# Performance work log

Measured on AMD Instinct MI355X. Metric: run time of the kernel, lower is better.

The kernel has to match this reference:

```python
import jax, jax.numpy as jnp
import numpy as np

N = 8192        # num nodes (bs in the original docstring)
D_IN = 512      # input feature dim
HEADS = 8
DPH = 512 // HEADS  # size_per_head = hidden_size // num_heads
EDGE_P = 0.01   # adjacency density


def setup_inputs() -> dict:
    key = jax.random.key(0)
    k1, k2, k3 = jax.random.split(key, 3)
    H = jax.random.normal(k1, (N, D_IN), dtype=jnp.float32)
    # dense 0/1 adjacency, as passed to the layer before tf.sparse.from_dense
    adj = (jax.random.uniform(k2, (N, N)) < EDGE_P).astype(jnp.float32)
    # Glorot-uniform per-head projection kernels, stacked: (HEADS, D_IN, DPH)
    limit = float(np.sqrt(6.0 / (D_IN + DPH)))
    W = jax.random.uniform(k3, (HEADS, D_IN, DPH), jnp.float32, -limit, limit)
    b = jnp.zeros((HEADS, DPH), jnp.float32)
    return {"H": H, "adj": adj, "W": W, "b": b}


def reference(H, adj, W, b):
    # Per-head dense projection: H_ = H @ W_h  -> (HEADS, N, DPH)
    H_ = jnp.einsum('nd,hde->hne', H, W)
    # NOTE: the original layer computes a sparse sigmoid/softmax attention
    # (f1 + f2^T over adj) but never uses it: head_output uses raw adj.
    # Aggregation: adj @ H_ per head, plus bias; activation = tf.identity.
    out = jnp.einsum('nm,hme->hne', adj, H_) + b[:, None, :]  # (HEADS, N, DPH)
    # Concat heads along feature axis (head 0 first) -> (N, HEADS*DPH)
    return jnp.transpose(out, (1, 0, 2)).reshape(H.shape[0], HEADS * DPH)
```

## Files before the change

### kernel.cpp

```cpp
#include <hip/hip_runtime.h>
#include <hip/hip_bf16.h>

typedef __attribute__((ext_vector_type(8))) short short8;
typedef __attribute__((ext_vector_type(4))) float floatx4;
typedef __attribute__((ext_vector_type(4))) uint uintx4;

#define GN 8192
#define GD 512
#define GEMM_BLOCKS 512

static __device__ __forceinline__ ushort bf16bits(float x) {
  __hip_bfloat16 h = __float2bfloat16(x);
  return *(ushort*)&h;
}
static __device__ __forceinline__ float bf16f(uint u16) {
  return __uint_as_float(u16 << 16);
}

typedef __attribute__((address_space(1))) const void g1_void;
typedef __attribute__((address_space(3))) void l3_void;
static __device__ __forceinline__ void gl_lds16(const void* g, void* l) {
  __builtin_amdgcn_global_load_lds((g1_void*)g, (l3_void*)l, 16, 0, 0);
}

__global__ void detect_kernel(const uint* __restrict__ H, const uint* __restrict__ W,
                              const uint* __restrict__ adj, const uint* __restrict__ b,
                              int* __restrict__ flags, float* __restrict__ bias) {
  __shared__ int cH, cW, cA, cB;
  const int t = threadIdx.x;
  if (t == 0) { cH = 0; cW = 0; cA = 0; cB = 0; }
  __syncthreads();
  { const uint e = (H[t] >> 7) & 0xFFu; if (e >= 100u && e <= 140u) atomicAdd(&cH, 1); }
  { const uint e = (W[t] >> 7) & 0xFFu; if (e >= 100u && e <= 140u) atomicAdd(&cW, 1); }
  for (int i = t; i < 4096; i += 256)
    if ((adj[i] & 0xFFFFu) == 0x3F80u) atomicAdd(&cA, 1);
  if (b[t] != 0u) atomicAdd(&cB, 1);
  __syncthreads();
  const int hb = cH > 128, wb = cW > 128, ab = cA > 0;
  if (t == 0) { flags[0] = hb; flags[1] = wb; flags[2] = ab; }
  if (cB == 0) {
    bias[t] = 0.0f; bias[t + 256] = 0.0f;
  } else if (wb) {
    const ushort* bs = (const ushort*)b;
    bias[t] = bf16f(bs[t]); bias[t + 256] = bf16f(bs[t + 256]);
  } else {
    const float* bf = (const float*)b;
    bias[t] = bf[t]; bias[t + 256] = bf[t + 256];
  }
}

#define BM 128
#define BN 64
#define BK 64
#define LDK 72

#define SMEM_BYTES (BM * LDK * 2 + BN * LDK * 2)

__global__ __launch_bounds__(256) void proj_kernel(
    const void* __restrict__ Hv, const void* __restrict__ Wv,
    ushort* __restrict__ HPt, const int* __restrict__ flags) {
  __shared__ __align__(16) unsigned char smem[SMEM_BYTES];
  ushort* sA = (ushort*)smem;
  ushort* sB = (ushort*)(smem + BM * LDK * 2);
  const int tid = threadIdx.x;
  const int hb = flags[0];
  const int wb = flags[1];
  const int bn = blockIdx.x & 7;
  const int bm = blockIdx.x >> 3;
  const int m0 = bm * BM;
  const int lane = tid & 63;
  const int w = tid >> 6;
  const int wr = w >> 1, wc = w & 1;
  const int l15 = lane & 15, q = lane >> 4;

  floatx4 acc[4][2];
#pragma unroll
  for (int i = 0; i < 4; i++)
#pragma unroll
    for (int j = 0; j < 2; j++) acc[i][j] = (floatx4)0.0f;

  for (int k0 = 0; k0 < GD; k0 += BK) {
    __syncthreads();
    if (hb) {
      const ushort* H16 = (const ushort*)Hv;
      const int r = tid >> 3;
      const int kc = (tid & 7) * 8;
#pragma unroll
      for (int p = 0; p < 4; p++) {
        const int row = r + p * 32;
        const uint4 v = *(const uint4*)(H16 + (size_t)(m0 + row) * GD + k0 + kc);
        *(uint4*)(sA + row * LDK + kc) = v;
      }
    } else {
      const float* H32 = (const float*)Hv;
      const int r0 = tid >> 4;
      const int kc = (tid & 15) * 4;
#pragma unroll
      for (int p = 0; p < 8; p++) {
        const int row = r0 + p * 16;
        const float4 v = *(const float4*)(H32 + (size_t)(m0 + row) * GD + k0 + kc);
        ushort4 o;
        o.x = bf16bits(v.x); o.y = bf16bits(v.y);
        o.z = bf16bits(v.z); o.w = bf16bits(v.w);
        *(ushort4*)(sA + row * LDK + kc) = o;
      }
    }
    if (wb) {
      const ushort* Wh = (const ushort*)Wv + (size_t)bn * (512 * 64);
      const int kk = tid >> 3;
      const int e0 = (tid & 7) * 8;
#pragma unroll
      for (int p = 0; p < 2; p++) {
        const int k = kk + p * 32;
        const uint4 v = *(const uint4*)(Wh + (size_t)(k0 + k) * 64 + e0);
        const ushort* pv = (const ushort*)&v;
#pragma unroll
        for (int j = 0; j < 8; j++) sB[(e0 + j) * LDK + k] = pv[j];
      }
    } else {
      const float* Wh = (const float*)Wv + (size_t)bn * (512 * 64);
      const int kk = tid >> 4;
      const int e0 = (tid & 15) * 4;
#pragma unroll
      for (int p = 0; p < 4; p++) {
        const int k = kk + p * 16;
        const float4 v = *(const float4*)(Wh + (size_t)(k0 + k) * 64 + e0);
        sB[(e0 + 0) * LDK + k] = bf16bits(v.x);
        sB[(e0 + 1) * LDK + k] = bf16bits(v.y);
        sB[(e0 + 2) * LDK + k] = bf16bits(v.z);
        sB[(e0 + 3) * LDK + k] = bf16bits(v.w);
      }
    }
    __syncthreads();
#pragma unroll
    for (int kq = 0; kq < 2; kq++) {
      short8 af[4], bfv[2];
#pragma unroll
      for (int mt = 0; mt < 4; mt++)
        af[mt] = *(const short8*)(sA + (wr * 64 + mt * 16 + l15) * LDK + kq * 32 + q * 8);
#pragma unroll
      for (int ct = 0; ct < 2; ct++)
        bfv[ct] = *(const short8*)(sB + (wc * 32 + ct * 16 + l15) * LDK + kq * 32 + q * 8);
#pragma unroll
      for (int mt = 0; mt < 4; mt++)
#pragma unroll
        for (int ct = 0; ct < 2; ct++)
          acc[mt][ct] = __builtin_amdgcn_mfma_f32_16x16x32_bf16(
              af[mt], bfv[ct], acc[mt][ct], 0, 0, 0);
    }
  }
#pragma unroll
  for (int mt = 0; mt < 4; mt++)
#pragma unroll
    for (int ct = 0; ct < 2; ct++) {
      const int col = bn * 64 + wc * 32 + ct * 16 + l15;
      const int rowb = m0 + wr * 64 + mt * 16 + q * 4;
      ushort4 o;
      o.x = bf16bits(acc[mt][ct][0]);
      o.y = bf16bits(acc[mt][ct][1]);
      o.z = bf16bits(acc[mt][ct][2]);
      o.w = bf16bits(acc[mt][ct][3]);
      *(ushort4*)(HPt + (size_t)col * GN + rowb) = o;
    }
}

#define ABM 64
#define ABK 64
#define AKCH 4096
#define ALDA 72

__global__ __launch_bounds__(512) void agg_kernel(
    const void* __restrict__ adjv, const ushort* __restrict__ HPt,
    float* __restrict__ pbuf, const int* __restrict__ flags) {
  __shared__ __align__(16) ushort sA[ABM * ALDA];
  __shared__ __align__(16) ushort sB[GD * 64];
  const int ab = flags[2];
  const int bid = blockIdx.x;
  const int kch = bid & 1;
  const int m0 = (bid >> 1) * ABM;
  const size_t kb = (size_t)kch * AKCH;
  const int tid = threadIdx.x;
  const int lane = tid & 63, w = tid >> 6;
  const int l15 = lane & 15, q = lane >> 4;

  floatx4 acc[4][4];
#pragma unroll
  for (int i = 0; i < 4; i++)
#pragma unroll
    for (int j = 0; j < 4; j++) acc[i][j] = (floatx4)0.0f;

  const int be0 = w * 8 + (lane >> 3);
  const int bkc = (lane & 7) * 8;

  for (int k0 = 0; k0 < AKCH; k0 += ABK) {
    __syncthreads();
#pragma unroll
    for (int p = 0; p < 8; p++) {
      const int e = p * 64 + be0;
      gl_lds16(HPt + (size_t)e * GN + kb + k0 + bkc,
               sB + (size_t)(p * 64 + w * 8) * 64);
    }
    if (ab) {
      const ushort* adj16 = (const ushort*)adjv;
      const int n = tid >> 3;
      const int kc = (tid & 7) * 8;
      const uintx4 v = __builtin_nontemporal_load(
          (const uintx4*)(adj16 + (size_t)(m0 + n) * GN + kb + k0 + kc));
      *(uintx4*)(sA + n * ALDA + kc) = v;
    } else {
      const float* adj32 = (const float*)adjv;
      const int n = tid >> 3;
      const int kc = (tid & 7) * 8;
      const float* src = adj32 + (size_t)(m0 + n) * GN + kb + k0 + kc;
      const floatx4 v0 = __builtin_nontemporal_load((const floatx4*)src);
      const floatx4 v1 = __builtin_nontemporal_load((const floatx4*)(src + 4));
      ushort4 o0, o1;
      o0.x = bf16bits(v0.x); o0.y = bf16bits(v0.y);
      o0.z = bf16bits(v0.z); o0.w = bf16bits(v0.w);
      o1.x = bf16bits(v1.x); o1.y = bf16bits(v1.y);
      o1.z = bf16bits(v1.z); o1.w = bf16bits(v1.w);
      *(ushort4*)(sA + n * ALDA + kc) = o0;
      *(ushort4*)(sA + n * ALDA + kc + 4) = o1;
    }
    __syncthreads();
#pragma unroll
    for (int kq = 0; kq < 2; kq++) {
      short8 af[4], bfr[4];
#pragma unroll
      for (int mt = 0; mt < 4; mt++)
        af[mt] = *(const short8*)(sA + (mt * 16 + l15) * ALDA + kq * 32 + q * 8);
#pragma unroll
      for (int ct = 0; ct < 4; ct++)
        bfr[ct] = *(const short8*)(sB + (w * 64 + ct * 16 + l15) * 64 + kq * 32 + q * 8);
#pragma unroll
      for (int mt = 0; mt < 4; mt++)
#pragma unroll
        for (int ct = 0; ct < 4; ct++)
          acc[mt][ct] = __builtin_amdgcn_mfma_f32_16x16x32_bf16(
              af[mt], bfr[ct], acc[mt][ct], 0, 0, 0);
    }
  }
  float* pb = pbuf + (size_t)kch * ((size_t)GN * GD);
#pragma unroll
  for (int mt = 0; mt < 4; mt++)
#pragma unroll
    for (int ct = 0; ct < 4; ct++) {
      const int col = w * 64 + ct * 16 + l15;
      const int rowb = m0 + mt * 16 + q * 4;
#pragma unroll
      for (int r = 0; r < 4; r++)
        pb[(size_t)(rowb + r) * GD + col] = acc[mt][ct][r];
    }
}

__global__ __launch_bounds__(256) void combine_kernel(
    const float* __restrict__ p0, const float* __restrict__ p1,
    const float* __restrict__ bias, float* __restrict__ out) {
  const int i = blockIdx.x * 256 + threadIdx.x;
  const floatx4 a = __builtin_nontemporal_load((const floatx4*)p0 + i);
  const floatx4 b = __builtin_nontemporal_load((const floatx4*)p1 + i);
  const floatx4 bb = *((const floatx4*)bias + (i & 127));
  floatx4 o;
  o.x = a.x + b.x + bb.x;
  o.y = a.y + b.y + bb.y;
  o.z = a.z + b.z + bb.z;
  o.w = a.w + b.w + bb.w;
  __builtin_nontemporal_store(o, (floatx4*)out + i);
}

extern "C" void kernel_launch(void* const* d_in, const int* in_sizes, int n_in,
                              void* d_out, int out_size, void* d_ws, size_t ws_size,
                              hipStream_t stream) {
  const void *H = d_in[0], *adj = d_in[1], *W = d_in[2], *b = d_in[3];
  for (int i = 0; i < n_in; i++) {
    const int s = in_sizes[i];
    if (s == GN * GN) adj = d_in[i];
    else if (s == GN * GD) H = d_in[i];
    else if (s == 8 * 512 * 64) W = d_in[i];
    else if (s == 512) b = d_in[i];
  }
  float* out = (float*)d_out;

  char* ws = (char*)d_ws;
  ushort* HPt  = (ushort*)ws;
  float*  bias = (float*)(ws + (size_t)GN * GD * 2);
  int*    flags= (int*)(ws + (size_t)GN * GD * 2 + 4096);
  float*  pbuf = (float*)(ws + (size_t)16 * 1024 * 1024);

  detect_kernel<<<1, 256, 0, stream>>>((const uint*)H, (const uint*)W,
                                       (const uint*)adj, (const uint*)b,
                                       flags, bias);
  proj_kernel<<<GEMM_BLOCKS, 256, 0, stream>>>(H, W, HPt, flags);
  agg_kernel<<<256, 512, 0, stream>>>(adj, HPt, pbuf, flags);
  combine_kernel<<<4096, 256, 0, stream>>>(pbuf, pbuf + (size_t)GN * GD, bias, out);
}
```

Before: 504.3 us.

## Split aggregation K into four chunks and XOR-swizzle the B tile in LDS

The aggregation GEMM now splits the reduction dimension into four chunks instead of two, launching 512 blocks rather than 256 so more CUs are busy. The combine kernel sums four partial buffers instead of two. The HPt tile loaded into LDS is XOR-swizzled on write and read to cut LDS bank conflicts, and partial results are stored nontemporally. In exchange, partial-buffer traffic doubles (four fp32 N×D buffers written and read back), and the workspace must be large enough to hold them.

```diff
diff --git a/kernel.cpp b/kernel.cpp
--- a/kernel.cpp
+++ b/kernel.cpp
@@ -166,7 +166,7 @@
 
 #define ABM 64
 #define ABK 64
-#define AKCH 4096
+#define AKCH 2048
 #define ALDA 72
 
 __global__ __launch_bounds__(512) void agg_kernel(
@@ -176,8 +176,8 @@
   __shared__ __align__(16) ushort sB[GD * 64];
   const int ab = flags[2];
   const int bid = blockIdx.x;
-  const int kch = bid & 1;
-  const int m0 = (bid >> 1) * ABM;
+  const int kch = bid & 3;
+  const int m0 = (bid >> 2) * ABM;
   const size_t kb = (size_t)kch * AKCH;
   const int tid = threadIdx.x;
   const int lane = tid & 63, w = tid >> 6;
@@ -189,14 +189,14 @@
 #pragma unroll
     for (int j = 0; j < 4; j++) acc[i][j] = (floatx4)0.0f;
 
-  const int be0 = w * 8 + (lane >> 3);
-  const int bkc = (lane & 7) * 8;
+  const int brow = lane >> 3;
+  const int bkc = ((lane & 7) ^ brow) * 8;
 
   for (int k0 = 0; k0 < AKCH; k0 += ABK) {
     __syncthreads();
 #pragma unroll
     for (int p = 0; p < 8; p++) {
-      const int e = p * 64 + be0;
+      const int e = p * 64 + w * 8 + brow;
       gl_lds16(HPt + (size_t)e * GN + kb + k0 + bkc,
                sB + (size_t)(p * 64 + w * 8) * 64);
     }
@@ -230,8 +230,11 @@
       for (int mt = 0; mt < 4; mt++)
         af[mt] = *(const short8*)(sA + (mt * 16 + l15) * ALDA + kq * 32 + q * 8);
 #pragma unroll
-      for (int ct = 0; ct < 4; ct++)
-        bfr[ct] = *(const short8*)(sB + (w * 64 + ct * 16 + l15) * 64 + kq * 32 + q * 8);
+      for (int ct = 0; ct < 4; ct++) {
+        const int r = w * 64 + ct * 16 + l15;
+        const int slot = (kq * 4 + q) ^ (l15 & 7);
+        bfr[ct] = *(const short8*)(sB + r * 64 + slot * 8);
+      }
 #pragma unroll
       for (int mt = 0; mt < 4; mt++)
 #pragma unroll
@@ -249,22 +252,26 @@
       const int rowb = m0 + mt * 16 + q * 4;
 #pragma unroll
       for (int r = 0; r < 4; r++)
-        pb[(size_t)(rowb + r) * GD + col] = acc[mt][ct][r];
+        __builtin_nontemporal_store(
+            acc[mt][ct][r], pb + (size_t)(rowb + r) * GD + col);
     }
 }
 
 __global__ __launch_bounds__(256) void combine_kernel(
-    const float* __restrict__ p0, const float* __restrict__ p1,
-    const float* __restrict__ bias, float* __restrict__ out) {
+    const float* __restrict__ pbuf, const float* __restrict__ bias,
+    float* __restrict__ out) {
   const int i = blockIdx.x * 256 + threadIdx.x;
-  const floatx4 a = __builtin_nontemporal_load((const floatx4*)p0 + i);
-  const floatx4 b = __builtin_nontemporal_load((const floatx4*)p1 + i);
+  const size_t stride = (size_t)GN * GD / 4;
+  floatx4 s = __builtin_nontemporal_load((const floatx4*)pbuf + i);
+#pragma unroll
+  for (int j = 1; j < 4; j++) {
+    const floatx4 a = __builtin_nontemporal_load(
+        (const floatx4*)pbuf + j * stride + i);
+    s.x += a.x; s.y += a.y; s.z += a.z; s.w += a.w;
+  }
   const floatx4 bb = *((const floatx4*)bias + (i & 127));
   floatx4 o;
-  o.x = a.x + b.x + bb.x;
-  o.y = a.y + b.y + bb.y;
-  o.z = a.z + b.z + bb.z;
-  o.w = a.w + b.w + bb.w;
+  o.x = s.x + bb.x; o.y = s.y + bb.y; o.z = s.z + bb.z; o.w = s.w + bb.w;
   __builtin_nontemporal_store(o, (floatx4*)out + i);
 }
 
@@ -291,6 +298,6 @@
                                        (const uint*)adj, (const uint*)b,
                                        flags, bias);
   proj_kernel<<<GEMM_BLOCKS, 256, 0, stream>>>(H, W, HPt, flags);
-  agg_kernel<<<256, 512, 0, stream>>>(adj, HPt, pbuf, flags);
-  combine_kernel<<<4096, 256, 0, stream>>>(pbuf, pbuf + (size_t)GN * GD, bias, out);
-}
+  agg_kernel<<<512, 512, 0, stream>>>(adj, HPt, pbuf, flags);
+  combine_kernel<<<4096, 256, 0, stream>>>(pbuf, bias, out);
+}
```

After: 514.1 us. Within noise of the previous version (+1.9%).
